# Kernel tuning notes

Hardware: AMD Instinct MI355X
Metric: run time of the kernel (lower is better)

Reference implementation:

```python
import jax, jax.numpy as jnp
import numpy as np

LN_EPS = 1e-5


def setup_inputs() -> dict:
    key = jax.random.key(0)
    ks = jax.random.split(key, 10)
    B, T, S, C = 8, 1024, 2048, 1024
    sd = 1.0 / np.sqrt(C)
    return {
        "x": jax.random.normal(ks[0], (B, T, C), jnp.float32),
        "lfb_feats": jax.random.normal(ks[1], (B, S, C), jnp.float32),
        "theta_w": jax.random.normal(ks[2], (C, C), jnp.float32) * sd,
        "theta_b": jax.random.normal(ks[3], (C,), jnp.float32) * 0.01,
        "phi_w": jax.random.normal(ks[4], (C, C), jnp.float32) * sd,
        "phi_b": jax.random.normal(ks[5], (C,), jnp.float32) * 0.01,
        "gi_w": jax.random.normal(ks[6], (C, C), jnp.float32) * sd,
        "gi_b": jax.random.normal(ks[7], (C,), jnp.float32) * 0.01,
        "ln_g": jnp.ones((C,), jnp.float32),
        "ln_b": jnp.zeros((C,), jnp.float32),
        "fc_w": jax.random.normal(ks[8], (C, C), jnp.float32) * sd,
        "fc_b": jax.random.normal(ks[9], (C,), jnp.float32) * 0.01,
    }


def _layernorm(h, g, b):
    mu = jnp.mean(h, axis=-1, keepdims=True)
    var = jnp.var(h, axis=-1, keepdims=True)
    return (h - mu) * jax.lax.rsqrt(var + LN_EPS) * g + b


def reference(x, lfb_feats, theta_w, theta_b, phi_w, phi_b, gi_w, gi_b,
              ln_g, ln_b, fc_w, fc_b):
    # x: [B,T,C], lfb_feats: [B,S,C]. 1x1 Conv1d == per-token linear on channels.
    C = x.shape[-1]
    scale = jnp.sqrt(jnp.asarray(C, x.dtype))  # NOTE: 1/sqrt(1/C) = sqrt(C) (as in source)
    theta = jnp.einsum('btc,oc->bto', x, theta_w) + theta_b          # [B,T,C]
    phi = jnp.einsum('bsc,oc->bso', lfb_feats, phi_w) + phi_b        # [B,S,C]
    gi = jnp.einsum('bsc,oc->bso', lfb_feats, gi_w) + gi_b           # [B,S,C]
    attn = jax.nn.softmax(jnp.einsum('btc,bsc->bts', theta, phi) * scale, axis=-1)
    out = jnp.einsum('bts,bsc->btc', attn, gi)                       # [B,T,C]
    out = jax.nn.relu(_layernorm(out, ln_g, ln_b))
    out = jnp.einsum('btc,oc->bto', out, fc_w) + fc_b                # fc (dropout = identity at eval)
    return out + x                                                   # residual, [B,T,C]
```

## Files before the change

### kernel.cpp

```cpp
#include <hip/hip_runtime.h>


#define BM 128
#define BN 128
#define BK 64

typedef __attribute__((ext_vector_type(8))) short short8;
typedef __attribute__((ext_vector_type(4))) float f32x4;
typedef __attribute__((ext_vector_type(4))) unsigned short us4;

enum { MODE_SPLIT = 0, MODE_TRANS = 1, MODE_F32 = 2, MODE_FINAL = 3 };

__device__ __forceinline__ float b2f(unsigned short u) {
  union { unsigned int i; float f; } x;
  x.i = ((unsigned int)u) << 16;
  return x.f;
}
__device__ __forceinline__ unsigned short f2b(float f) {
  unsigned int u = __float_as_uint(f);
  unsigned int r = (u + 0x7FFFu + ((u >> 16) & 1u)) >> 16;
  return (unsigned short)r;
}

__device__ __forceinline__ void async_cp16(const unsigned short* g,
                                           unsigned short* l) {
  __builtin_amdgcn_global_load_lds(
      (const __attribute__((address_space(1))) void*)g,
      (__attribute__((address_space(3))) void*)l, 16, 0, 0);
}

__global__ __launch_bounds__(256) void split_xlfb(
    const float* __restrict__ lfb, const float* __restrict__ x,
    const float* __restrict__ g, unsigned short* __restrict__ ls,
    unsigned short* __restrict__ xs, float* __restrict__ v, int Ms) {
  const int id = blockIdx.x;
  const int t = threadIdx.x;
  const int c = t * 4;
  if (id < Ms) {
    __shared__ float red[4];
    f32x4 xv = *(const f32x4*)&lfb[(size_t)id * 1024 + c];
    f32x4 gg = *(const f32x4*)&g[c];
    us4 hi, lo;
    float s = 0.f;
#pragma unroll
    for (int i = 0; i < 4; ++i) {
      hi[i] = f2b(xv[i]);
      lo[i] = f2b(xv[i] - b2f(hi[i]));
      s += xv[i] * gg[i];
    }
    *(us4*)&ls[(size_t)id * 2048 + c] = hi;
    *(us4*)&ls[(size_t)id * 2048 + 1024 + c] = lo;
    for (int o = 32; o; o >>= 1) s += __shfl_xor(s, o, 64);
    if ((t & 63) == 0) red[t >> 6] = s;
    __syncthreads();
    if (t == 0) v[id] = red[0] + red[1] + red[2] + red[3];
  } else {
    const int r = id - Ms;
    f32x4 xv = *(const f32x4*)&x[(size_t)r * 1024 + c];
    us4 hi, lo;
#pragma unroll
    for (int i = 0; i < 4; ++i) {
      hi[i] = f2b(xv[i]);
      lo[i] = f2b(xv[i] - b2f(hi[i]));
    }
    *(us4*)&xs[(size_t)r * 2048 + c] = hi;
    *(us4*)&xs[(size_t)r * 2048 + 1024 + c] = lo;
  }
}

__global__ __launch_bounds__(256) void cvt2_bf16(const float* __restrict__ s0,
                                                 unsigned short* __restrict__ d0,
                                                 const float* __restrict__ s1,
                                                 unsigned short* __restrict__ d1) {
  int b = blockIdx.x;
  const float* src = (b < 1024) ? s0 : s1;
  unsigned short* dst = (b < 1024) ? d0 : d1;
  int g = (b & 1023) * 256 + threadIdx.x;
  f32x4 v = *(const f32x4*)&src[g * 4];
  us4 o;
#pragma unroll
  for (int i = 0; i < 4; ++i) o[i] = f2b(v[i]);
  *(us4*)&dst[(size_t)g * 4] = o;
}

__global__ __launch_bounds__(256) void transpose_split2(
    const float* __restrict__ W0, unsigned short* __restrict__ T0,
    const float* __restrict__ W1, unsigned short* __restrict__ T1) {
  __shared__ float tile[64][65];
  const int sel = blockIdx.y >> 4;
  const float* W = sel ? W1 : W0;
  unsigned short* T = sel ? T1 : T0;
  const int bo = (blockIdx.y & 15) * 64;
  const int bc = blockIdx.x * 64;
  const int t = threadIdx.x;
  const int tr = t >> 4;
  const int tc = (t & 15) * 4;
#pragma unroll
  for (int i = 0; i < 4; ++i) {
    f32x4 v = *(const f32x4*)&W[(size_t)(bo + tr + 16 * i) * 1024 + bc + tc];
#pragma unroll
    for (int j = 0; j < 4; ++j) tile[tr + 16 * i][tc + j] = v[j];
  }
  __syncthreads();
#pragma unroll
  for (int i = 0; i < 4; ++i) {
    const int c = bc + tr + 16 * i;
    us4 hi, lo;
#pragma unroll
    for (int j = 0; j < 4; ++j) {
      float v = tile[tc + j][tr + 16 * i];
      hi[j] = f2b(v);
      lo[j] = f2b(v - b2f(hi[j]));
    }
    *(us4*)&T[(size_t)c * 2048 + bo + tc] = hi;
    *(us4*)&T[(size_t)c * 2048 + 1024 + bo + tc] = lo;
  }
}

__global__ __launch_bounds__(256) void make_g(
    const unsigned short* __restrict__ tB, const float* __restrict__ bth,
    float* __restrict__ g) {
  const int d = blockIdx.x * 4 + (threadIdx.x >> 6);
  const int lane = threadIdx.x & 63;
  float s = 0.f;
#pragma unroll
  for (int i = 0; i < 4; ++i) {
    const int o0 = lane * 4 + i * 256;
    us4 h = *(const us4*)&tB[(size_t)d * 2048 + o0];
    us4 lo = *(const us4*)&tB[(size_t)d * 2048 + 1024 + o0];
    f32x4 bb = *(const f32x4*)&bth[o0];
#pragma unroll
    for (int j = 0; j < 4; ++j) s += (b2f(h[j]) + b2f(lo[j])) * bb[j];
  }
  for (int o = 32; o; o >>= 1) s += __shfl_xor(s, o, 64);
  if (lane == 0) g[d] = s;
}

__global__ __launch_bounds__(256) void reduce_g(const float* __restrict__ P,
                                                unsigned short* __restrict__ Gs) {
  const int d = blockIdx.x;
  const int c = threadIdx.x * 4;
  f32x4 s = *(const f32x4*)&P[(size_t)d * 1024 + c];
#pragma unroll
  for (int z = 1; z < 8; ++z) {
    f32x4 p = *(const f32x4*)&P[(size_t)z * 1048576 + (size_t)d * 1024 + c];
#pragma unroll
    for (int i = 0; i < 4; ++i) s[i] += p[i];
  }
  us4 hi, lo;
#pragma unroll
  for (int i = 0; i < 4; ++i) {
    hi[i] = f2b(s[i]);
    lo[i] = f2b(s[i] - b2f(hi[i]));
  }
  *(us4*)&Gs[(size_t)d * 2048 + c] = hi;
  *(us4*)&Gs[(size_t)d * 2048 + 1024 + c] = lo;
}

template <int MODE>
__global__ __launch_bounds__(256, 4) void gemm_bt(
    const unsigned short* __restrict__ A, const unsigned short* __restrict__ B,
    void* __restrict__ Cout, const float* __restrict__ bias,
    const float* __restrict__ resid, int M, int N, int K, int lda, int ldb,
    int ldc, long long sA, long long sB, long long sC, long long sBias,
    int awrap, int awoff, int bwrap, int bwoff, int NBk, int MBk, int mbx,
    int swz, int kzoff) {
  __shared__ __align__(16) unsigned short As[BM * BK];
  __shared__ __align__(16) unsigned short Bs[BN * BK];

  const int tid = threadIdx.x;
  const int l = tid & 63;
  const int w = tid >> 6;
  const int wm = w >> 1, wn = w & 1;
  const int ln = l & 15, lq = l >> 4;

  int bmi, bni, bzi;
  {
    const int id = blockIdx.x;
    if (swz == 1) {
      bzi = id & 7;
      const int r = id >> 3;
      bmi = r % mbx;
      bni = r / mbx;
    } else if (swz == 2) {
      bzi = 0;
      const int r = id >> 3;
      bmi = (id & 7) * mbx + r % mbx;
      bni = r / mbx;
    } else {
      bni = id % NBk;
      const int rem = id / NBk;
      bmi = rem % MBk;
      bzi = rem / MBk;
    }
  }
  const int bm = bmi * BM;
  const int bn = bni * BN;
  const unsigned short* Ab = A + (size_t)bzi * (size_t)sA;
  const unsigned short* Bb = B + (size_t)bzi * (size_t)sB;
  const float* bz = bias ? bias + (size_t)bzi * (size_t)sBias : nullptr;
  const int kbase = bzi * kzoff;

  const int arow = tid >> 3;
  const int acol = (((tid & 7) ^ ((tid >> 3) & 7)) * 8);
  const int ldsbase = (tid & 0xC0) * 8;

  f32x4 acc[4][4];
#pragma unroll
  for (int i = 0; i < 4; ++i)
#pragma unroll
    for (int j = 0; j < 4; ++j) acc[i][j] = (f32x4){0.f, 0.f, 0.f, 0.f};

  const int sw = ln & 7;

  for (int k0 = 0; k0 < K; k0 += BK) {
    const int kg = k0 + kbase;
    const int ka = (kg < awrap) ? kg : kg - awoff;
    const int kb = (kg < bwrap) ? kg : kg - bwoff;
#pragma unroll
    for (int it = 0; it < 4; ++it) {
      const int r = it * 32 + arow;
      async_cp16(Ab + (size_t)(bm + r) * lda + ka + acol,
                 &As[it * 2048 + ldsbase]);
    }
#pragma unroll
    for (int it = 0; it < 4; ++it) {
      const int r = it * 32 + arow;
      async_cp16(Bb + (size_t)(bn + r) * ldb + kb + acol,
                 &Bs[it * 2048 + ldsbase]);
    }
    __syncthreads();

#pragma unroll
    for (int ks = 0; ks < 2; ++ks) {
      short8 a[4], b[4];
      const int kof = ((ks * 4 + lq) ^ sw) * 8;
#pragma unroll
      for (int i = 0; i < 4; ++i)
        a[i] = *(const short8*)&As[(wm * 64 + i * 16 + ln) * BK + kof];
#pragma unroll
      for (int j = 0; j < 4; ++j)
        b[j] = *(const short8*)&Bs[(wn * 64 + j * 16 + ln) * BK + kof];
#pragma unroll
      for (int i = 0; i < 4; ++i)
#pragma unroll
        for (int j = 0; j < 4; ++j)
          acc[i][j] = __builtin_amdgcn_mfma_f32_16x16x32_bf16(a[i], b[j],
                                                              acc[i][j], 0, 0, 0);
    }
    __syncthreads();
  }

  float* Cf = (float*)Cout + (size_t)bzi * (size_t)sC;
  unsigned short* Cb = (unsigned short*)Cout + (size_t)bzi * (size_t)sC;

  if constexpr (MODE == MODE_TRANS) {
#pragma unroll
    for (int i = 0; i < 4; ++i) {
      const int gm0 = bm + wm * 64 + i * 16 + lq * 4;
      const int bt = gm0 >> 11;
      const int sr = gm0 & 2047;
#pragma unroll
      for (int j = 0; j < 4; ++j) {
        const int gn = bn + wn * 64 + j * 16 + ln;
        const float bv2 = (bz != nullptr) ? bz[gn] : 0.f;
        us4 o;
#pragma unroll
        for (int r = 0; r < 4; ++r) o[r] = f2b(acc[i][j][r] + bv2);
        *(us4*)&Cb[(size_t)bt * 2097152 + (size_t)gn * 2048 + sr] = o;
      }
    }
  } else {
#pragma unroll
    for (int j = 0; j < 4; ++j) {
      const int gn = bn + wn * 64 + j * 16 + ln;
      const float bv2 = (bz != nullptr) ? bz[gn] : 0.f;
#pragma unroll
      for (int i = 0; i < 4; ++i) {
        const int gm0 = bm + wm * 64 + i * 16 + lq * 4;
#pragma unroll
        for (int r = 0; r < 4; ++r) {
          const int gm = gm0 + r;
          const float v = acc[i][j][r] + bv2;
          if constexpr (MODE == MODE_SPLIT) {
            unsigned short hi = f2b(v);
            Cb[(size_t)gm * ldc + gn] = hi;
            Cb[(size_t)gm * ldc + gn + (ldc >> 1)] = f2b(v - b2f(hi));
          } else if constexpr (MODE == MODE_F32) {
            Cf[(size_t)gm * ldc + gn] = v;
          } else if constexpr (MODE == MODE_FINAL) {
            const size_t idx = (size_t)gm * ldc + gn;
            Cf[idx] = v + resid[idx];
          }
        }
      }
    }
  }
}

__device__ __forceinline__ void ld8f(const unsigned short* Lb, int roff, int ln,
                                     int lq, int sw, short8* a) {
#pragma unroll
  for (int mi = 0; mi < 4; ++mi)
#pragma unroll
    for (int ks = 0; ks < 2; ++ks)
      a[mi * 2 + ks] = *(const short8*)&Lb[(roff + mi * 16 + ln) * 64 +
                                           (((ks * 4 + lq) ^ sw) * 8)];
}
__device__ __forceinline__ void ld4f(const unsigned short* Lb, int roff, int ln,
                                     int lq, int sw, short8* b) {
#pragma unroll
  for (int ni = 0; ni < 2; ++ni)
#pragma unroll
    for (int ks = 0; ks < 2; ++ks)
      b[ni * 2 + ks] = *(const short8*)&Lb[(roff + ni * 16 + ln) * 64 +
                                           (((ks * 4 + lq) ^ sw) * 8)];
}
template <int MH, int NH>
__device__ __forceinline__ void mfmaQ(f32x4 (&acc)[8][4], const short8* a,
                                      const short8* b) {
  __builtin_amdgcn_s_setprio(1);
#pragma unroll
  for (int mi = 0; mi < 4; ++mi)
#pragma unroll
    for (int ni = 0; ni < 2; ++ni)
#pragma unroll
      for (int ks = 0; ks < 2; ++ks)
        acc[MH * 4 + mi][NH * 2 + ni] = __builtin_amdgcn_mfma_f32_16x16x32_bf16(
            a[mi * 2 + ks], b[ni * 2 + ks], acc[MH * 4 + mi][NH * 2 + ni], 0, 0,
            0);
  __builtin_amdgcn_s_setprio(0);
}

template <int MODE>
__global__ __launch_bounds__(512, 1) void gemm8(
    const unsigned short* __restrict__ A, const unsigned short* __restrict__ B,
    void* __restrict__ Cout, const float* __restrict__ bias, int M, int N,
    int K, int lda, int ldb, int ldc, long long sA, long long sB, long long sC,
    long long sBias, int awrap, int awoff, int bwrap, int bwoff, int NBk,
    int MBk, int mbx, int swz) {
  __shared__ __align__(16) unsigned short Abuf[2][2][8192];
  __shared__ __align__(16) unsigned short Bbuf[2][2][8192];

  const int tid = threadIdx.x;
  const int l = tid & 63;
  const int w = tid >> 6;
  const int wm = w >> 2;
  const int wn = w & 3;
  const int ln = l & 15, lq = l >> 4;
  const int sw = ln & 7;

  int bmi, bni, bzi;
  {
    const int id = blockIdx.x;
    if (swz == 1) {
      bzi = id & 7;
      const int r = id >> 3;
      bmi = r % mbx;
      bni = r / mbx;
    } else if (swz == 2) {
      bzi = 0;
      const int r = id >> 3;
      bmi = (id & 7) * mbx + r % mbx;
      bni = r / mbx;
    } else {
      bni = id % NBk;
      const int rem = id / NBk;
      bmi = rem % MBk;
      bzi = rem / MBk;
    }
  }
  const int bm = bmi * 256;
  const int bn = bni * 256;
  const unsigned short* Ab = A + (size_t)bzi * (size_t)sA;
  const unsigned short* Bb = B + (size_t)bzi * (size_t)sB;
  const float* bz = bias ? bias + (size_t)bzi * (size_t)sBias : nullptr;

  const int srow = tid >> 3;
  const int schk = ((tid & 7) ^ ((tid >> 3) & 7)) * 8;
  const int sdst0 = (tid & 448) * 8;

  auto stageA = [&](int d, int kk) {
#pragma unroll
    for (int half = 0; half < 2; ++half)
#pragma unroll
      for (int j = 0; j < 2; ++j)
        async_cp16(Ab + (size_t)(bm + half * 128 + srow + j * 64) * lda + kk +
                       schk,
                   &Abuf[d][half][sdst0 + j * 4096]);
  };
  auto stageB = [&](int d, int kk) {
#pragma unroll
    for (int half = 0; half < 2; ++half)
#pragma unroll
      for (int j = 0; j < 2; ++j)
        async_cp16(Bb + (size_t)(bn + half * 128 + srow + j * 64) * ldb + kk +
                       schk,
                   &Bbuf[d][half][sdst0 + j * 4096]);
  };
  auto wrapA = [&](int kg) { return (kg < awrap) ? kg : kg - awoff; };
  auto wrapB = [&](int kg) { return (kg < bwrap) ? kg : kg - bwoff; };

  f32x4 acc[8][4];
#pragma unroll
  for (int i = 0; i < 8; ++i)
#pragma unroll
    for (int j = 0; j < 4; ++j) acc[i][j] = (f32x4){0.f, 0.f, 0.f, 0.f};

  const int nt = K >> 6;

  stageA(0, wrapA(0));
  stageB(0, wrapB(0));
  if (nt > 1) {
    stageB(1, wrapB(64));
    asm volatile("s_waitcnt vmcnt(4)" : : : "memory");
  } else {
    asm volatile("s_waitcnt vmcnt(0)" : : : "memory");
  }
  __builtin_amdgcn_sched_barrier(0);
  __builtin_amdgcn_s_barrier();

  short8 a0[8], a1[8], b0[4], b1[4];
  const int broff = (wn & 1) * 64;
  const int bhalf = wn >> 1;

  for (int t = 0; t < nt; ++t) {
    const int p = t & 1;
    const unsigned short* LA = &Abuf[p][wm][0];
    const unsigned short* LB = &Bbuf[p][bhalf][0];
    ld8f(LA, 0, ln, lq, sw, a0);
    ld4f(LB, broff, ln, lq, sw, b0);
    ld4f(LB, broff + 32, ln, lq, sw, b1);
    ld8f(LA, 64, ln, lq, sw, a1);
    if (t + 1 < nt) stageA(p ^ 1, wrapA((t + 1) * 64));
    mfmaQ<0, 0>(acc, a0, b0);
    mfmaQ<0, 1>(acc, a0, b1);
    __builtin_amdgcn_s_barrier();
    if (t + 2 < nt) stageB(p, wrapB((t + 2) * 64));
    mfmaQ<1, 1>(acc, a1, b1);
    mfmaQ<1, 0>(acc, a1, b0);
    if (t + 2 < nt) {
      asm volatile("s_waitcnt vmcnt(4)" : : : "memory");
    } else {
      asm volatile("s_waitcnt vmcnt(0)" : : : "memory");
    }
    __builtin_amdgcn_sched_barrier(0);
    __builtin_amdgcn_s_barrier();
  }

  float* Cf = (float*)Cout + (size_t)bzi * (size_t)sC;
  unsigned short* Cb = (unsigned short*)Cout;

  if constexpr (MODE == MODE_TRANS) {
#pragma unroll
    for (int mi = 0; mi < 8; ++mi) {
      const int gm0 = bm + wm * 128 + mi * 16 + lq * 4;
      const int bt = gm0 >> 11;
      const int sr = gm0 & 2047;
#pragma unroll
      for (int ni = 0; ni < 4; ++ni) {
        const int gn = bn + wn * 64 + ni * 16 + ln;
        const float bv2 = (bz != nullptr) ? bz[gn] : 0.f;
        us4 o;
#pragma unroll
        for (int r = 0; r < 4; ++r) o[r] = f2b(acc[mi][ni][r] + bv2);
        *(us4*)&Cb[(size_t)bt * 2097152 + (size_t)gn * 2048 + sr] = o;
      }
    }
  } else {
#pragma unroll
    for (int ni = 0; ni < 4; ++ni) {
      const int gn = bn + wn * 64 + ni * 16 + ln;
      const float bv2 = (bz != nullptr) ? bz[gn] : 0.f;
#pragma unroll
      for (int mi = 0; mi < 8; ++mi) {
        const int gm0 = bm + wm * 128 + mi * 16 + lq * 4;
#pragma unroll
        for (int r = 0; r < 4; ++r)
          Cf[(size_t)(gm0 + r) * ldc + gn] = acc[mi][ni][r] + bv2;
      }
    }
  }
}

__global__ __launch_bounds__(256) void softmax_rows(
    const float* __restrict__ logit, unsigned short* __restrict__ attn) {
  const int row = blockIdx.x;
  const float* L = logit + (size_t)row * 2048;
  unsigned short* O = attn + (size_t)row * 2048;
  const int t = threadIdx.x;
  __shared__ float red[8];

  f32x4 v0 = *(const f32x4*)&L[t * 4];
  f32x4 v1 = *(const f32x4*)&L[t * 4 + 1024];
  float m = fmaxf(fmaxf(fmaxf(v0[0], v0[1]), fmaxf(v0[2], v0[3])),
                  fmaxf(fmaxf(v1[0], v1[1]), fmaxf(v1[2], v1[3])));
  for (int o = 32; o; o >>= 1) m = fmaxf(m, __shfl_xor(m, o, 64));
  if ((t & 63) == 0) red[t >> 6] = m;
  __syncthreads();
  m = fmaxf(fmaxf(red[0], red[1]), fmaxf(red[2], red[3]));

  float e[8];
  float s = 0.f;
#pragma unroll
  for (int i = 0; i < 4; ++i) { e[i] = __expf(32.f * (v0[i] - m)); s += e[i]; }
#pragma unroll
  for (int i = 0; i < 4; ++i) { e[4 + i] = __expf(32.f * (v1[i] - m)); s += e[4 + i]; }
  for (int o = 32; o; o >>= 1) s += __shfl_xor(s, o, 64);
  if ((t & 63) == 0) red[4 + (t >> 6)] = s;
  __syncthreads();
  s = red[4] + red[5] + red[6] + red[7];
  const float inv = 1.f / s;
  us4 o0, o1;
#pragma unroll
  for (int i = 0; i < 4; ++i) { o0[i] = f2b(e[i] * inv); o1[i] = f2b(e[4 + i] * inv); }
  *(us4*)&O[t * 4] = o0;
  *(us4*)&O[t * 4 + 1024] = o1;
}

__global__ __launch_bounds__(256) void ln_relu(
    const float* __restrict__ X, const float* __restrict__ g,
    const float* __restrict__ b, unsigned short* __restrict__ H) {
  const int row = blockIdx.x;
  const float* x = X + (size_t)row * 1024;
  unsigned short* h = H + (size_t)row * 1024;
  const int t = threadIdx.x;
  __shared__ float red[8];
  f32x4 v = *(const f32x4*)&x[t * 4];
  float s = v[0] + v[1] + v[2] + v[3];
  float q = v[0] * v[0] + v[1] * v[1] + v[2] * v[2] + v[3] * v[3];
  for (int o = 32; o; o >>= 1) {
    s += __shfl_xor(s, o, 64);
    q += __shfl_xor(q, o, 64);
  }
  if ((t & 63) == 0) { red[t >> 6] = s; red[4 + (t >> 6)] = q; }
  __syncthreads();
  s = red[0] + red[1] + red[2] + red[3];
  q = red[4] + red[5] + red[6] + red[7];
  const float mean = s * (1.f / 1024.f);
  const float var = q * (1.f / 1024.f) - mean * mean;
  const float rstd = rsqrtf(var + 1e-5f);
  us4 o;
#pragma unroll
  for (int i = 0; i < 4; ++i) {
    const int c = t * 4 + i;
    const float y = (v[i] - mean) * rstd * g[c] + b[c];
    o[i] = f2b(fmaxf(y, 0.f));
  }
  *(us4*)&h[t * 4] = o;
}

extern "C" void kernel_launch(void* const* d_in, const int* in_sizes, int n_in,
                              void* d_out, int out_size, void* d_ws,
                              size_t ws_size, hipStream_t stream) {
  const float* x = (const float*)d_in[0];
  const float* lfb = (const float*)d_in[1];
  const float* th_w = (const float*)d_in[2];
  const float* th_b = (const float*)d_in[3];
  const float* ph_w = (const float*)d_in[4];
  const float* gi_w = (const float*)d_in[6];
  const float* gi_b = (const float*)d_in[7];
  const float* lng = (const float*)d_in[8];
  const float* lnb = (const float*)d_in[9];
  const float* fc_w = (const float*)d_in[10];
  const float* fc_b = (const float*)d_in[11];
  float* outf = (float*)d_out;
  char* ws = (char*)d_ws;

  const size_t MB = 1048576;
  int nb = 1;
  for (int cand = 8; cand >= 1; cand >>= 1)
    if ((size_t)cand * 24 * MB + 18 * MB <= ws_size) { nb = cand; break; }

  char* tail = ws + (size_t)nb * 24 * MB;
  unsigned short* tA = (unsigned short*)(tail);
  unsigned short* tB = (unsigned short*)(tail + 4 * MB);
  unsigned short* Gs = (unsigned short*)(tail + 8 * MB);
  unsigned short* giw = (unsigned short*)(tail + 12 * MB);
  unsigned short* fcw = (unsigned short*)(tail + 14 * MB);
  float* gv = (float*)(tail + 16 * MB);
  float* vb = (float*)(tail + 16 * MB + 65536);

  dim3 blk(256);
  transpose_split2<<<dim3(16, 32), blk, 0, stream>>>(th_w, tA, ph_w, tB);
  make_g<<<dim3(256), blk, 0, stream>>>(tB, th_b, gv);
  if (nb >= 2) {
    float* gpart = (float*)ws;
    gemm_bt<MODE_F32><<<dim3(512), blk, 0, stream>>>(
        tB, tA, gpart, nullptr, nullptr, 1024, 1024, 384, 2048, 2048, 1024,
        0, 0, 1048576LL, 0, 2048, 2048, 1024, 1024, 8, 8, 8, 1, 384);
    reduce_g<<<dim3(1024), blk, 0, stream>>>(gpart, Gs);
  } else {
    gemm_bt<MODE_SPLIT><<<dim3(64), blk, 0, stream>>>(
        tB, tA, Gs, nullptr, nullptr, 1024, 1024, 3072, 2048, 2048, 2048,
        0, 0, 0, 0, 2048, 2048, 1024, 1024, 8, 8, 1, 2, 0);
  }
  cvt2_bf16<<<dim3(2048), blk, 0, stream>>>(gi_w, giw, fc_w, fcw);

  for (int b0 = 0; b0 < 8; b0 += nb) {
    unsigned short* xs = (unsigned short*)(ws);
    float* logit = (float*)(ws);
    unsigned short* ls = (unsigned short*)(ws + (size_t)nb * 8 * MB);
    unsigned short* ys = (unsigned short*)(ws + (size_t)nb * 16 * MB);
    unsigned short* giT = (unsigned short*)(ws + (size_t)nb * 20 * MB);
    unsigned short* attn = ys;
    float* outp = (float*)ws;
    unsigned short* h = giT;

    const float* xb = x + (size_t)b0 * 1048576;
    const float* lfbb = lfb + (size_t)b0 * 2097152;
    float* ob = outf + (size_t)b0 * 1048576;
    const int Ms = nb * 2048;
    const int Mt = nb * 1024;
    const int zswz = (nb == 8) ? 1 : 0;

    split_xlfb<<<dim3(Ms + Mt), blk, 0, stream>>>(lfbb, xb, gv, ls, xs, vb, Ms);
    gemm8<MODE_TRANS><<<dim3(32 * nb), dim3(512), 0, stream>>>(
        ls, giw, giT, gi_b, Ms, 1024, 1024, 2048, 1024, 2048,
        0LL, 0LL, 0LL, 0LL, 1024, 0, 1024, 0, 4, 8 * nb, nb, 2);
    gemm_bt<MODE_SPLIT><<<dim3(8 * (Mt / 128)), blk, 0, stream>>>(
        xs, Gs, ys, nullptr, nullptr, Mt, 1024, 3072, 2048, 2048, 2048,
        0, 0, 0, 0, 2048, 2048, 1024, 1024, 8, Mt / 128, Mt / 1024, 2, 0);
    gemm8<MODE_F32><<<dim3(32 * nb), dim3(512), 0, stream>>>(
        ys, ls, logit, vb, 1024, 2048, 3072, 2048, 2048, 2048,
        2097152LL, 4194304LL, 2097152LL, 2048LL, 2048, 2048, 1024, 1024,
        8, 4, 4, zswz);
    softmax_rows<<<dim3(Mt), blk, 0, stream>>>(logit, attn);
    gemm_bt<MODE_F32><<<dim3(8 * 8 * nb), blk, 0, stream>>>(
        attn, giT, outp, nullptr, nullptr, 1024, 1024, 2048, 2048, 2048, 1024,
        2097152LL, 2097152LL, 1048576LL, 0, 2048, 0, 2048, 0, 8, 8, 8, zswz, 0);
    ln_relu<<<dim3(Mt), blk, 0, stream>>>(outp, lng, lnb, h);
    gemm_bt<MODE_FINAL><<<dim3(8 * (Mt / 128)), blk, 0, stream>>>(
        h, fcw, ob, fc_b, xb, Mt, 1024, 1024, 1024, 1024, 1024,
        0, 0, 0, 0, 1024, 0, 1024, 0, 8, Mt / 128, Mt / 1024, 2, 0);
  }
}
```

Baseline: 502.7 us.

## Use 4 waves with 128x128 per-wave tiles in 256x256 gemm8 kernel

Changes the gemm8 block from 8 waves (each covering 128x64 of the 256x256 tile) to 4 waves each covering 128x128. Staging loops are reworked so 256 threads move the same tiles, and the accumulator array doubles to 8x8. The aim is more LDS fragment reuse per MFMA and fewer LDS reads per wave. In exchange, register pressure rises sharply (256 accumulator floats plus 32 fragment registers), occupancy drops, and an explicit lgkmcnt wait is added mid-iteration.

```diff
diff --git a/kernel.cpp b/kernel.cpp
--- a/kernel.cpp
+++ b/kernel.cpp
@@ -298,42 +298,13 @@
   }
 }
 
-__device__ __forceinline__ void ld8f(const unsigned short* Lb, int roff, int ln,
-                                     int lq, int sw, short8* a) {
-#pragma unroll
-  for (int mi = 0; mi < 4; ++mi)
-#pragma unroll
-    for (int ks = 0; ks < 2; ++ks)
-      a[mi * 2 + ks] = *(const short8*)&Lb[(roff + mi * 16 + ln) * 64 +
-                                           (((ks * 4 + lq) ^ sw) * 8)];
-}
-__device__ __forceinline__ void ld4f(const unsigned short* Lb, int roff, int ln,
-                                     int lq, int sw, short8* b) {
-#pragma unroll
-  for (int ni = 0; ni < 2; ++ni)
-#pragma unroll
-    for (int ks = 0; ks < 2; ++ks)
-      b[ni * 2 + ks] = *(const short8*)&Lb[(roff + ni * 16 + ln) * 64 +
-                                           (((ks * 4 + lq) ^ sw) * 8)];
-}
-template <int MH, int NH>
-__device__ __forceinline__ void mfmaQ(f32x4 (&acc)[8][4], const short8* a,
-                                      const short8* b) {
-  __builtin_amdgcn_s_setprio(1);
-#pragma unroll
-  for (int mi = 0; mi < 4; ++mi)
-#pragma unroll
-    for (int ni = 0; ni < 2; ++ni)
-#pragma unroll
-      for (int ks = 0; ks < 2; ++ks)
-        acc[MH * 4 + mi][NH * 2 + ni] = __builtin_amdgcn_mfma_f32_16x16x32_bf16(
-            a[mi * 2 + ks], b[ni * 2 + ks], acc[MH * 4 + mi][NH * 2 + ni], 0, 0,
-            0);
-  __builtin_amdgcn_s_setprio(0);
+__device__ __forceinline__ short8 ldfrag(const unsigned short* Lb, int f,
+                                         int ks, int ln, int lq, int sw) {
+  return *(const short8*)&Lb[(f * 16 + ln) * 64 + (((ks * 4 + lq) ^ sw) * 8)];
 }
 
 template <int MODE>
-__global__ __launch_bounds__(512, 1) void gemm8(
+__global__ __launch_bounds__(256, 1) void gemm8(
     const unsigned short* __restrict__ A, const unsigned short* __restrict__ B,
     void* __restrict__ Cout, const float* __restrict__ bias, int M, int N,
     int K, int lda, int ldb, int ldc, long long sA, long long sB, long long sC,
@@ -345,8 +316,8 @@
   const int tid = threadIdx.x;
   const int l = tid & 63;
   const int w = tid >> 6;
-  const int wm = w >> 2;
-  const int wn = w & 3;
+  const int wm = w >> 1;
+  const int wn = w & 1;
   const int ln = l & 15, lq = l >> 4;
   const int sw = ln & 7;
 
@@ -378,34 +349,34 @@
 
   const int srow = tid >> 3;
   const int schk = ((tid & 7) ^ ((tid >> 3) & 7)) * 8;
-  const int sdst0 = (tid & 448) * 8;
+  const int dstoff = tid * 8;
 
   auto stageA = [&](int d, int kk) {
 #pragma unroll
     for (int half = 0; half < 2; ++half)
 #pragma unroll
-      for (int j = 0; j < 2; ++j)
-        async_cp16(Ab + (size_t)(bm + half * 128 + srow + j * 64) * lda + kk +
+      for (int j = 0; j < 4; ++j)
+        async_cp16(Ab + (size_t)(bm + half * 128 + j * 32 + srow) * lda + kk +
                        schk,
-                   &Abuf[d][half][sdst0 + j * 4096]);
+                   &Abuf[d][half][j * 2048 + dstoff]);
   };
   auto stageB = [&](int d, int kk) {
 #pragma unroll
     for (int half = 0; half < 2; ++half)
 #pragma unroll
-      for (int j = 0; j < 2; ++j)
-        async_cp16(Bb + (size_t)(bn + half * 128 + srow + j * 64) * ldb + kk +
+      for (int j = 0; j < 4; ++j)
+        async_cp16(Bb + (size_t)(bn + half * 128 + j * 32 + srow) * ldb + kk +
                        schk,
-                   &Bbuf[d][half][sdst0 + j * 4096]);
+                   &Bbuf[d][half][j * 2048 + dstoff]);
   };
   auto wrapA = [&](int kg) { return (kg < awrap) ? kg : kg - awoff; };
   auto wrapB = [&](int kg) { return (kg < bwrap) ? kg : kg - bwoff; };
 
-  f32x4 acc[8][4];
+  f32x4 acc[8][8];
 #pragma unroll
   for (int i = 0; i < 8; ++i)
 #pragma unroll
-    for (int j = 0; j < 4; ++j) acc[i][j] = (f32x4){0.f, 0.f, 0.f, 0.f};
+    for (int j = 0; j < 8; ++j) acc[i][j] = (f32x4){0.f, 0.f, 0.f, 0.f};
 
   const int nt = K >> 6;
 
@@ -413,34 +384,51 @@
   stageB(0, wrapB(0));
   if (nt > 1) {
     stageB(1, wrapB(64));
-    asm volatile("s_waitcnt vmcnt(4)" : : : "memory");
+    asm volatile("s_waitcnt vmcnt(8)" : : : "memory");
   } else {
     asm volatile("s_waitcnt vmcnt(0)" : : : "memory");
   }
   __builtin_amdgcn_sched_barrier(0);
   __builtin_amdgcn_s_barrier();
 
-  short8 a0[8], a1[8], b0[4], b1[4];
-  const int broff = (wn & 1) * 64;
-  const int bhalf = wn >> 1;
+  short8 a0[8], b0[8], a1[8], b1[8];
 
   for (int t = 0; t < nt; ++t) {
     const int p = t & 1;
     const unsigned short* LA = &Abuf[p][wm][0];
-    const unsigned short* LB = &Bbuf[p][bhalf][0];
-    ld8f(LA, 0, ln, lq, sw, a0);
-    ld4f(LB, broff, ln, lq, sw, b0);
-    ld4f(LB, broff + 32, ln, lq, sw, b1);
-    ld8f(LA, 64, ln, lq, sw, a1);
+    const unsigned short* LB = &Bbuf[p][wn][0];
+#pragma unroll
+    for (int f = 0; f < 8; ++f) a0[f] = ldfrag(LA, f, 0, ln, lq, sw);
+#pragma unroll
+    for (int f = 0; f < 8; ++f) b0[f] = ldfrag(LB, f, 0, ln, lq, sw);
+#pragma unroll
+    for (int f = 0; f < 8; ++f) a1[f] = ldfrag(LA, f, 1, ln, lq, sw);
+#pragma unroll
+    for (int f = 0; f < 8; ++f) b1[f] = ldfrag(LB, f, 1, ln, lq, sw);
     if (t + 1 < nt) stageA(p ^ 1, wrapA((t + 1) * 64));
-    mfmaQ<0, 0>(acc, a0, b0);
-    mfmaQ<0, 1>(acc, a0, b1);
+    __builtin_amdgcn_s_setprio(1);
+#pragma unroll
+    for (int i = 0; i < 8; ++i)
+#pragma unroll
+      for (int j = 0; j < 8; ++j)
+        acc[i][j] =
+            __builtin_amdgcn_mfma_f32_16x16x32_bf16(a0[i], b0[j], acc[i][j],
+                                                    0, 0, 0);
+    __builtin_amdgcn_s_setprio(0);
+    asm volatile("s_waitcnt lgkmcnt(0)" : : : "memory");
     __builtin_amdgcn_s_barrier();
     if (t + 2 < nt) stageB(p, wrapB((t + 2) * 64));
-    mfmaQ<1, 1>(acc, a1, b1);
-    mfmaQ<1, 0>(acc, a1, b0);
+    __builtin_amdgcn_s_setprio(1);
+#pragma unroll
+    for (int i = 0; i < 8; ++i)
+#pragma unroll
+      for (int j = 0; j < 8; ++j)
+        acc[i][j] =
+            __builtin_amdgcn_mfma_f32_16x16x32_bf16(a1[i], b1[j], acc[i][j],
+                                                    0, 0, 0);
+    __builtin_amdgcn_s_setprio(0);
     if (t + 2 < nt) {
-      asm volatile("s_waitcnt vmcnt(4)" : : : "memory");
+      asm volatile("s_waitcnt vmcnt(8)" : : : "memory");
     } else {
       asm volatile("s_waitcnt vmcnt(0)" : : : "memory");
     }
@@ -458,8 +446,8 @@
       const int bt = gm0 >> 11;
       const int sr = gm0 & 2047;
 #pragma unroll
-      for (int ni = 0; ni < 4; ++ni) {
-        const int gn = bn + wn * 64 + ni * 16 + ln;
+      for (int ni = 0; ni < 8; ++ni) {
+        const int gn = bn + wn * 128 + ni * 16 + ln;
         const float bv2 = (bz != nullptr) ? bz[gn] : 0.f;
         us4 o;
 #pragma unroll
@@ -469,8 +457,8 @@
     }
   } else {
 #pragma unroll
-    for (int ni = 0; ni < 4; ++ni) {
-      const int gn = bn + wn * 64 + ni * 16 + ln;
+    for (int ni = 0; ni < 8; ++ni) {
+      const int gn = bn + wn * 128 + ni * 16 + ln;
       const float bv2 = (bz != nullptr) ? bz[gn] : 0.f;
 #pragma unroll
       for (int mi = 0; mi < 8; ++mi) {
@@ -615,13 +603,13 @@
     const int zswz = (nb == 8) ? 1 : 0;
 
     split_xlfb<<<dim3(Ms + Mt), blk, 0, stream>>>(lfbb, xb, gv, ls, xs, vb, Ms);
-    gemm8<MODE_TRANS><<<dim3(32 * nb), dim3(512), 0, stream>>>(
+    gemm8<MODE_TRANS><<<dim3(32 * nb), dim3(256), 0, stream>>>(
         ls, giw, giT, gi_b, Ms, 1024, 1024, 2048, 1024, 2048,
         0LL, 0LL, 0LL, 0LL, 1024, 0, 1024, 0, 4, 8 * nb, nb, 2);
     gemm_bt<MODE_SPLIT><<<dim3(8 * (Mt / 128)), blk, 0, stream>>>(
         xs, Gs, ys, nullptr, nullptr, Mt, 1024, 3072, 2048, 2048, 2048,
         0, 0, 0, 0, 2048, 2048, 1024, 1024, 8, Mt / 128, Mt / 1024, 2, 0);
-    gemm8<MODE_F32><<<dim3(32 * nb), dim3(512), 0, stream>>>(
+    gemm8<MODE_F32><<<dim3(32 * nb), dim3(256), 0, stream>>>(
         ys, ls, logit, vb, 1024, 2048, 3072, 2048, 2048, 2048,
         2097152LL, 4194304LL, 2097152LL, 2048LL, 2048, 2048, 1024, 1024,
         8, 4, 4, zswz);
```

Result: no change. 503.6 us (+0.2%).

## Add 256x128 eight-wave GEMM kernel and route three GEMMs through it

Applied to the files above, without the earlier changes.

Adds gemm8B, a 512-thread kernel that computes a 256x128 output tile per block with double-buffered async LDS staging, swizzled loads and s_setprio around the MFMA bursts. The theta/split GEMM, the attn·gi GEMM and the final fc GEMM now use it in place of the 256-thread 128x128 gemm_bt, which raises operand reuse per block and cuts the block count. It also adds an explicit lgkmcnt(0) wait before the mid-loop barrier in the existing gemm8. The trade-offs are higher LDS and register use per block, which can lower occupancy, and fewer blocks for small batches.

```diff
diff --git a/kernel.cpp b/kernel.cpp
--- a/kernel.cpp
+++ b/kernel.cpp
@@ -435,6 +435,7 @@
     if (t + 1 < nt) stageA(p ^ 1, wrapA((t + 1) * 64));
     mfmaQ<0, 0>(acc, a0, b0);
     mfmaQ<0, 1>(acc, a0, b1);
+    asm volatile("s_waitcnt lgkmcnt(0)" : : : "memory");
     __builtin_amdgcn_s_barrier();
     if (t + 2 < nt) stageB(p, wrapB((t + 2) * 64));
     mfmaQ<1, 1>(acc, a1, b1);
@@ -478,6 +479,169 @@
 #pragma unroll
         for (int r = 0; r < 4; ++r)
           Cf[(size_t)(gm0 + r) * ldc + gn] = acc[mi][ni][r] + bv2;
+      }
+    }
+  }
+}
+
+template <int MODE>
+__global__ __launch_bounds__(512, 1) void gemm8B(
+    const unsigned short* __restrict__ A, const unsigned short* __restrict__ B,
+    void* __restrict__ Cout, const float* __restrict__ bias,
+    const float* __restrict__ resid, int M, int N, int K, int lda, int ldb,
+    int ldc, long long sA, long long sB, long long sC, long long sBias,
+    int awrap, int awoff, int bwrap, int bwoff, int NBk, int MBk, int mbx,
+    int swz) {
+  __shared__ __align__(16) unsigned short Abuf[2][2][8192];
+  __shared__ __align__(16) unsigned short Bbuf[2][8192];
+
+  const int tid = threadIdx.x;
+  const int l = tid & 63;
+  const int w = tid >> 6;
+  const int wm = w >> 1;
+  const int wn = w & 1;
+  const int ln = l & 15, lq = l >> 4;
+  const int sw = ln & 7;
+
+  int bmi, bni, bzi;
+  {
+    const int id = blockIdx.x;
+    if (swz == 1) {
+      bzi = id & 7;
+      const int r = id >> 3;
+      bmi = r % mbx;
+      bni = r / mbx;
+    } else if (swz == 2) {
+      bzi = 0;
+      const int r = id >> 3;
+      bmi = (id & 7) * mbx + r % mbx;
+      bni = r / mbx;
+    } else {
+      bni = id % NBk;
+      const int rem = id / NBk;
+      bmi = rem % MBk;
+      bzi = rem / MBk;
+    }
+  }
+  const int bm = bmi * 256;
+  const int bn = bni * 128;
+  const unsigned short* Ab = A + (size_t)bzi * (size_t)sA;
+  const unsigned short* Bb = B + (size_t)bzi * (size_t)sB;
+  const float* bz = bias ? bias + (size_t)bzi * (size_t)sBias : nullptr;
+
+  const int srow = tid >> 3;
+  const int schk = ((tid & 7) ^ ((tid >> 3) & 7)) * 8;
+  const int sdst0 = (tid & 448) * 8;
+
+  auto stageA = [&](int d, int kk) {
+#pragma unroll
+    for (int half = 0; half < 2; ++half)
+#pragma unroll
+      for (int j = 0; j < 2; ++j)
+        async_cp16(Ab + (size_t)(bm + half * 128 + srow + j * 64) * lda + kk +
+                       schk,
+                   &Abuf[d][half][sdst0 + j * 4096]);
+  };
+  auto stageB = [&](int d, int kk) {
+#pragma unroll
+    for (int j = 0; j < 2; ++j)
+      async_cp16(Bb + (size_t)(bn + srow + j * 64) * ldb + kk + schk,
+                 &Bbuf[d][sdst0 + j * 4096]);
+  };
+  auto wrapA = [&](int kg) { return (kg < awrap) ? kg : kg - awoff; };
+  auto wrapB = [&](int kg) { return (kg < bwrap) ? kg : kg - bwoff; };
+
+  f32x4 acc[4][4];
+#pragma unroll
+  for (int i = 0; i < 4; ++i)
+#pragma unroll
+    for (int j = 0; j < 4; ++j) acc[i][j] = (f32x4){0.f, 0.f, 0.f, 0.f};
+
+  const int nt = K >> 6;
+
+  stageA(0, wrapA(0));
+  stageB(0, wrapB(0));
+  if (nt > 1) {
+    stageB(1, wrapB(64));
+    asm volatile("s_waitcnt vmcnt(2)" : : : "memory");
+  } else {
+    asm volatile("s_waitcnt vmcnt(0)" : : : "memory");
+  }
+  __builtin_amdgcn_sched_barrier(0);
+  __builtin_amdgcn_s_barrier();
+
+  const int ahalf = wm >> 1;
+  const int aroff = (wm & 1) * 64;
+  const int broff = wn * 64;
+
+  for (int t = 0; t < nt; ++t) {
+    const int p = t & 1;
+    const unsigned short* LA = &Abuf[p][ahalf][0];
+    const unsigned short* LB = &Bbuf[p][0];
+    short8 a[2][4], b[2][4];
+#pragma unroll
+    for (int ks = 0; ks < 2; ++ks) {
+      const int kof = ((ks * 4 + lq) ^ sw) * 8;
+#pragma unroll
+      for (int i = 0; i < 4; ++i)
+        a[ks][i] = *(const short8*)&LA[(aroff + i * 16 + ln) * 64 + kof];
+#pragma unroll
+      for (int j = 0; j < 4; ++j)
+        b[ks][j] = *(const short8*)&LB[(broff + j * 16 + ln) * 64 + kof];
+    }
+    if (t + 1 < nt) stageA(p ^ 1, wrapA((t + 1) * 64));
+    __builtin_amdgcn_s_setprio(1);
+#pragma unroll
+    for (int i = 0; i < 4; ++i)
+#pragma unroll
+      for (int j = 0; j < 4; ++j)
+        acc[i][j] = __builtin_amdgcn_mfma_f32_16x16x32_bf16(a[0][i], b[0][j],
+                                                            acc[i][j], 0, 0, 0);
+    __builtin_amdgcn_s_setprio(0);
+    asm volatile("s_waitcnt lgkmcnt(0)" : : : "memory");
+    __builtin_amdgcn_s_barrier();
+    if (t + 2 < nt) stageB(p, wrapB((t + 2) * 64));
+    __builtin_amdgcn_s_setprio(1);
+#pragma unroll
+    for (int i = 0; i < 4; ++i)
+#pragma unroll
+      for (int j = 0; j < 4; ++j)
+        acc[i][j] = __builtin_amdgcn_mfma_f32_16x16x32_bf16(a[1][i], b[1][j],
+                                                            acc[i][j], 0, 0, 0);
+    __builtin_amdgcn_s_setprio(0);
+    if (t + 2 < nt) {
+      asm volatile("s_waitcnt vmcnt(2)" : : : "memory");
+    } else {
+      asm volatile("s_waitcnt vmcnt(0)" : : : "memory");
+    }
+    __builtin_amdgcn_sched_barrier(0);
+    __builtin_amdgcn_s_barrier();
+  }
+
+  float* Cf = (float*)Cout + (size_t)bzi * (size_t)sC;
+  unsigned short* Cb = (unsigned short*)Cout + (size_t)bzi * (size_t)sC;
+
+#pragma unroll
+  for (int j = 0; j < 4; ++j) {
+    const int gn = bn + wn * 64 + j * 16 + ln;
+    const float bv2 = (bz != nullptr) ? bz[gn] : 0.f;
+#pragma unroll
+    for (int i = 0; i < 4; ++i) {
+      const int gm0 = bm + wm * 64 + i * 16 + lq * 4;
+#pragma unroll
+      for (int r = 0; r < 4; ++r) {
+        const int gm = gm0 + r;
+        const float v = acc[i][j][r] + bv2;
+        if constexpr (MODE == MODE_SPLIT) {
+          unsigned short hi = f2b(v);
+          Cb[(size_t)gm * ldc + gn] = hi;
+          Cb[(size_t)gm * ldc + gn + (ldc >> 1)] = f2b(v - b2f(hi));
+        } else if constexpr (MODE == MODE_F32) {
+          Cf[(size_t)gm * ldc + gn] = v;
+        } else if constexpr (MODE == MODE_FINAL) {
+          const size_t idx = (size_t)gm * ldc + gn;
+          Cf[idx] = v + resid[idx];
+        }
       }
     }
   }
@@ -613,25 +777,28 @@
     const int Ms = nb * 2048;
     const int Mt = nb * 1024;
     const int zswz = (nb == 8) ? 1 : 0;
+    const int mswz = (nb == 8) ? 2 : 0;
 
     split_xlfb<<<dim3(Ms + Mt), blk, 0, stream>>>(lfbb, xb, gv, ls, xs, vb, Ms);
     gemm8<MODE_TRANS><<<dim3(32 * nb), dim3(512), 0, stream>>>(
         ls, giw, giT, gi_b, Ms, 1024, 1024, 2048, 1024, 2048,
         0LL, 0LL, 0LL, 0LL, 1024, 0, 1024, 0, 4, 8 * nb, nb, 2);
-    gemm_bt<MODE_SPLIT><<<dim3(8 * (Mt / 128)), blk, 0, stream>>>(
+    gemm8B<MODE_SPLIT><<<dim3((Mt / 256) * 8), dim3(512), 0, stream>>>(
         xs, Gs, ys, nullptr, nullptr, Mt, 1024, 3072, 2048, 2048, 2048,
-        0, 0, 0, 0, 2048, 2048, 1024, 1024, 8, Mt / 128, Mt / 1024, 2, 0);
+        0LL, 0LL, 0LL, 0LL, 2048, 2048, 1024, 1024, 8, Mt / 256,
+        (nb == 8) ? (Mt / 2048) : 0, mswz);
     gemm8<MODE_F32><<<dim3(32 * nb), dim3(512), 0, stream>>>(
         ys, ls, logit, vb, 1024, 2048, 3072, 2048, 2048, 2048,
         2097152LL, 4194304LL, 2097152LL, 2048LL, 2048, 2048, 1024, 1024,
         8, 4, 4, zswz);
     softmax_rows<<<dim3(Mt), blk, 0, stream>>>(logit, attn);
-    gemm_bt<MODE_F32><<<dim3(8 * 8 * nb), blk, 0, stream>>>(
+    gemm8B<MODE_F32><<<dim3(32 * nb), dim3(512), 0, stream>>>(
         attn, giT, outp, nullptr, nullptr, 1024, 1024, 2048, 2048, 2048, 1024,
-        2097152LL, 2097152LL, 1048576LL, 0, 2048, 0, 2048, 0, 8, 8, 8, zswz, 0);
+        2097152LL, 2097152LL, 1048576LL, 0LL, 2048, 0, 2048, 0, 8, 4, 4, zswz);
     ln_relu<<<dim3(Mt), blk, 0, stream>>>(outp, lng, lnb, h);
-    gemm_bt<MODE_FINAL><<<dim3(8 * (Mt / 128)), blk, 0, stream>>>(
+    gemm8B<MODE_FINAL><<<dim3((Mt / 256) * 8), dim3(512), 0, stream>>>(
         h, fcw, ob, fc_b, xb, Mt, 1024, 1024, 1024, 1024, 1024,
-        0, 0, 0, 0, 1024, 0, 1024, 0, 8, Mt / 128, Mt / 1024, 2, 0);
-  }
-}
+        0LL, 0LL, 0LL, 0LL, 1024, 0, 1024, 0, 8, Mt / 256,
+        (nb == 8) ? (Mt / 2048) : 0, mswz);
+  }
+}
```

Result: faster. 482.0 us (-4.1%).
